# Optimization experiments

Hardware: AMD Instinct MI355X
Metric: run time of the kernel (lower is better)

## Reference

```python
import jax, jax.numpy as jnp
import numpy as np

B, N, F, DEG = 64, 1024, 128, 8
K1, K2, K3 = 512, 256, 128  # ceil(0.5*N) cascaded pool sizes
NUM_CLASSES = 10
E = B * N * DEG

def _elu(x):
    return jnp.where(x > 0, x, jnp.expm1(x))

def gcn(x, W, b, src, dst, ev, n):
    # PyG GCNConv with improved=True: self-loop weight 2, symmetric norm
    h = x @ W
    w = ev.astype(h.dtype)
    deg = jax.ops.segment_sum(w, dst, num_segments=n) + 2.0
    dinv = jax.lax.rsqrt(deg)
    coef = (w * dinv[src] * dinv[dst])[:, None]
    out = jax.ops.segment_sum(h[src] * coef, dst, num_segments=n)
    out = out + h * (2.0 * dinv * dinv)[:, None]  # self-loop term
    return out + b

def topk_pool(x, p, src, dst, ev, bg, npg, k):
    # score = tanh(x.p/||p||); keep top-k per graph; mask+remap edges
    score = jnp.tanh((x @ p) / jnp.linalg.norm(p))
    vals, idx = jax.lax.top_k(score.reshape(bg, npg), k)
    perm = (idx + (jnp.arange(bg) * npg)[:, None]).reshape(-1)
    x_new = x[perm] * vals.reshape(-1)[:, None]
    remap = jnp.full((bg * npg,), -1, jnp.int32).at[perm].set(
        jnp.arange(bg * k, dtype=jnp.int32))
    s2, d2 = remap[src], remap[dst]
    ev2 = ev & (s2 >= 0) & (d2 >= 0)
    return x_new, jnp.maximum(s2, 0), jnp.maximum(d2, 0), ev2, perm

def setup_inputs() -> dict:
    key = jax.random.key(0)
    ks = jax.random.split(key, 16)
    offs = (jnp.arange(B) * N)[:, None]
    e_per = DEG * N
    src = (jax.random.randint(ks[0], (B, e_per), 0, N) + offs).reshape(-1).astype(jnp.int32)
    dst = (jax.random.randint(ks[1], (B, e_per), 0, N) + offs).reshape(-1).astype(jnp.int32)
    def w(k, shape, fan_in):
        return jax.random.normal(k, shape, jnp.float32) / np.sqrt(fan_in)
    return {
        "x": jax.random.normal(ks[2], (B * N, F), jnp.float32),
        "W1": w(ks[3], (F, 32), F), "b1": jnp.zeros((32,)), "p1": w(ks[4], (32,), 32),
        "W2": w(ks[5], (32, 64), 32), "b2": jnp.zeros((64,)), "p2": w(ks[6], (64,), 64),
        "W3": w(ks[7], (64, 128), 64), "b3": jnp.zeros((128,)), "p3": w(ks[8], (128,), 128),
        "W4": w(ks[9], (128, 256), 128), "b4": jnp.zeros((256,)),
        "W5": w(ks[10], (384, 128), 384), "b5": jnp.zeros((128,)),
        "W6": w(ks[11], (192, 64), 192), "b6": jnp.zeros((64,)),
        "W7": w(ks[12], (96, 32), 96), "b7": jnp.zeros((32,)),
        "Wl": w(ks[13], (64, 64), 64),
        "Wc": w(ks[14], (64, NUM_CLASSES), 64), "bc": jnp.zeros((NUM_CLASSES,)),
        "src": src, "dst": dst,
    }

def reference(x, W1, b1, p1, W2, b2, p2, W3, b3, p3, W4, b4,
              W5, b5, W6, b6, W7, b7, Wl, Wc, bc, src, dst):
    ev0 = jnp.ones((E,), bool)
    x1 = _elu(gcn(x, W1, b1, src, dst, ev0, B * N))
    x2, s2, d2, ev2, idx2 = topk_pool(x1, p1, src, dst, ev0, B, N, K1)
    x2 = _elu(x2)
    x3 = _elu(gcn(x2, W2, b2, s2, d2, ev2, B * K1))
    x4, s4, d4, ev4, idx4 = topk_pool(x3, p2, s2, d2, ev2, B, K1, K2)
    x4 = _elu(x4)
    x5 = _elu(gcn(x4, W3, b3, s4, d4, ev4, B * K2))
    x6, s6, d6, ev6, idx6 = topk_pool(x5, p3, s4, d4, ev4, B, K2, K3)
    x6 = _elu(x6)
    x7 = _elu(gcn(x6, W4, b4, s6, d6, ev6, B * K3))
    x8 = jnp.zeros((B * K2, 256), x7.dtype).at[idx6].set(x7)
    x8 = _elu(jnp.concatenate([x8, x5], axis=1))
    x9 = _elu(gcn(x8, W5, b5, s4, d4, ev4, B * K2))
    x10 = jnp.zeros((B * K1, 128), x9.dtype).at[idx4].set(x9)
    x10 = _elu(jnp.concatenate([x10, x3], axis=1))
    x11 = _elu(gcn(x10, W6, b6, s2, d2, ev2, B * K1))
    x12 = jnp.zeros((B * N, 64), x11.dtype).at[idx2].set(x11)
    x12 = _elu(jnp.concatenate([x12, x1], axis=1))
    x13 = _elu(gcn(x12, W7, b7, src, dst, ev0, B * N))
    batch = jnp.repeat(jnp.arange(B), N)
    gmp = jax.ops.segment_max(x13, batch, num_segments=B)
    gap = jax.ops.segment_sum(x13, batch, num_segments=B) / N
    g = _elu(jnp.concatenate([gmp, gap], axis=1))
    g = _elu(g @ Wl)
    logits = g @ Wc + bc
    return jax.nn.log_softmax(logits, axis=-1)
```

## Files before the change

kernel.cpp:

```cpp
#include <hip/hip_runtime.h>
#include <hip/hip_bf16.h>
#include <math.h>

#define B_ 64
#define N_ 1024
#define E_ 524288
#define K1_ 512
#define K2_ 256
#define K3_ 128
#define M0_ 65536
#define M1_ 32768
#define M2_ 16384
#define M3_ 8192

static __device__ __forceinline__ float eluf(float x){ return x > 0.f ? x : expm1f(x); }
static __device__ __forceinline__ float4 elu4(float4 v){
  float4 o; o.x=eluf(v.x); o.y=eluf(v.y); o.z=eluf(v.z); o.w=eluf(v.w); return o;
}

template<int BM,int BN,int MODE>
__global__ __launch_bounds__(256) void k_mm(const float* __restrict__ X,
    const float* __restrict__ W, float* __restrict__ H, int M, int K, int N,
    const int* __restrict__ perm, const float* __restrict__ vals,
    const float* __restrict__ Xd, const int* __restrict__ orig,
    const int* __restrict__ rm, int WD4){
  constexpr int TX = BN/4;
  constexpr int TY = 256/TX;
  constexpr int RM = BM/TY;
  __shared__ float Xs[BM][36];
  __shared__ float Ws[32][BN];
  const int t = threadIdx.x;
  const int tx = t % TX, ty = t / TX;
  const int m0 = blockIdx.x*BM, n0 = blockIdx.y*BN;
  float acc[RM][4];
  #pragma unroll
  for (int r=0;r<RM;++r){acc[r][0]=0.f;acc[r][1]=0.f;acc[r][2]=0.f;acc[r][3]=0.f;}
  for (int k0=0;k0<K;k0+=32){
    #pragma unroll
    for (int l=0;l<BM/32;++l){
      int fi=l*256+t, row=fi>>3, q=fi&7;
      int m = m0+row;
      int c4 = (k0>>2)+q;
      float4 v;
      if (MODE==0){
        v = *(const float4*)(X + (size_t)m*K + (c4<<2));
      } else if (MODE==1){
        int pm = perm[m]; float vv = vals[m];
        float4 h = *(const float4*)(X + (size_t)pm*K + (c4<<2));
        v.x=eluf(h.x*vv); v.y=eluf(h.y*vv); v.z=eluf(h.z*vv); v.w=eluf(h.w*vv);
      } else {
        if (c4 < WD4){
          int o = orig ? orig[m] : m;
          int j = rm[o];
          if (j>=0) v = elu4(*(const float4*)(Xd + ((size_t)j*WD4 + c4)*4));
          else { v.x=0.f;v.y=0.f;v.z=0.f;v.w=0.f; }
        } else {
          int ws4 = (K>>2) - WD4;
          v = elu4(*(const float4*)(X + ((size_t)m*ws4 + (c4-WD4))*4));
        }
      }
      *(float4*)(&Xs[row][q*4]) = v;
    }
    #pragma unroll
    for (int l=0;l<BN/32;++l){
      int fi=l*256+t, wrow=fi/(BN/4), wq=fi%(BN/4);
      *(float4*)(&Ws[wrow][wq*4]) = *(const float4*)(W + (size_t)(k0+wrow)*N + n0 + wq*4);
    }
    __syncthreads();
    #pragma unroll
    for (int kq=0;kq<32;kq+=4){
      float4 xv[RM];
      #pragma unroll
      for (int r=0;r<RM;++r) xv[r] = *(const float4*)(&Xs[ty*RM+r][kq]);
      #pragma unroll
      for (int j=0;j<4;++j){
        float4 wv = *(const float4*)(&Ws[kq+j][tx*4]);
        #pragma unroll
        for (int r=0;r<RM;++r){
          float xs = (j==0)?xv[r].x:(j==1)?xv[r].y:(j==2)?xv[r].z:xv[r].w;
          acc[r][0]=fmaf(xs,wv.x,acc[r][0]);
          acc[r][1]=fmaf(xs,wv.y,acc[r][1]);
          acc[r][2]=fmaf(xs,wv.z,acc[r][2]);
          acc[r][3]=fmaf(xs,wv.w,acc[r][3]);
        }
      }
    }
    __syncthreads();
  }
  #pragma unroll
  for (int r=0;r<RM;++r){
    int m = m0 + ty*RM + r;
    float4 h; h.x=acc[r][0];h.y=acc[r][1];h.z=acc[r][2];h.w=acc[r][3];
    *(float4*)(H + (size_t)m*N + n0 + tx*4) = h;
  }
}

__global__ void k_deg0(const int* __restrict__ dst, int* __restrict__ degi){
  int i = blockIdx.x*256+threadIdx.x; if (i>=E_) return;
  atomicAdd(&degi[dst[i]], 1);
}
__global__ void k_place0(const int* __restrict__ src, const int* __restrict__ dst,
                         int* __restrict__ cursor, int* __restrict__ col){
  int i = blockIdx.x*256+threadIdx.x; if (i>=E_) return;
  int p = atomicAdd(&cursor[dst[i]], 1);
  col[p] = src[i];
}

__global__ __launch_bounds__(256) void k_scanA(const int* __restrict__ degi,
                                               int* __restrict__ bsum){
  __shared__ int ls[256];
  int b = blockIdx.x, t = threadIdx.x;
  ls[t] = degi[b*256+t]; __syncthreads();
  for (int o=128;o>0;o>>=1){ if (t<o) ls[t]+=ls[t+o]; __syncthreads(); }
  if (t==0) bsum[b] = ls[0];
}
__global__ __launch_bounds__(256) void k_scanB(int* __restrict__ bsum){
  __shared__ int ps[256];
  int t = threadIdx.x;
  ps[t] = bsum[t]; __syncthreads();
  for (int o=1;o<256;o<<=1){
    int v = (t>=o) ? ps[t-o] : 0;
    __syncthreads(); ps[t]+=v; __syncthreads();
  }
  bsum[t] = ps[t];
}
__global__ __launch_bounds__(256) void k_scanC(const int* __restrict__ degi,
    const int* __restrict__ bsum, int* __restrict__ rowptr,
    int* __restrict__ cursor, float* __restrict__ dinv){
  __shared__ int ps[256];
  int b = blockIdx.x, t = threadIdx.x;
  int i = b*256+t;
  int d = degi[i];
  ps[t] = d; __syncthreads();
  for (int o=1;o<256;o<<=1){
    int v = (t>=o) ? ps[t-o] : 0;
    __syncthreads(); ps[t]+=v; __syncthreads();
  }
  int off = (b==0 ? 0 : bsum[b-1]) + ps[t] - d;
  rowptr[i] = off; cursor[i] = off;
  dinv[i] = rsqrtf((float)d + 2.f);
  if (i == M0_-1) rowptr[M0_] = off + d;
}

__global__ void k_deg_orig(const int* __restrict__ orig, const int* __restrict__ rowptr0,
                           const int* __restrict__ col0, const int* __restrict__ rm,
                           float* __restrict__ dinv, int M){
  int i = blockIdx.x*256+threadIdx.x; if (i>=M) return;
  int o = orig[i];
  int beg = rowptr0[o], end = rowptr0[o+1];
  int d = 0;
  for (int j=beg;j<end;++j) d += (rm[col0[j]] >= 0) ? 1 : 0;
  dinv[i] = rsqrtf((float)d + 2.f);
}

__global__ void k_compose_idx(const int* __restrict__ prevOrig, const int* __restrict__ idxL,
                              int* __restrict__ origL, int n){
  int i = blockIdx.x*256+threadIdx.x; if (i<n) origL[i] = prevOrig[idxL[i]];
}

template<int F, bool SCORE>
__global__ __launch_bounds__(256) void k_gather(const int* __restrict__ rowptr,
    const int* __restrict__ col, const float* __restrict__ dinv,
    const float* __restrict__ H, const float* __restrict__ bias,
    float* __restrict__ OUT, int M,
    const float* __restrict__ p, float* __restrict__ score){
  constexpr int FQ = F/4;
  int i = blockIdx.x*256+threadIdx.x;
  if (i >= M*FQ) return;
  int n = i/FQ, q = i - (i/FQ)*FQ;
  int beg = rowptr[n], end = rowptr[n+1];
  float4 acc; acc.x=0.f;acc.y=0.f;acc.z=0.f;acc.w=0.f;
  for (int j=beg;j<end;++j){
    int s = col[j];
    float c = dinv[s];
    float4 h = *(const float4*)(H + (size_t)s*F + q*4);
    acc.x=fmaf(c,h.x,acc.x); acc.y=fmaf(c,h.y,acc.y);
    acc.z=fmaf(c,h.z,acc.z); acc.w=fmaf(c,h.w,acc.w);
  }
  float dn = dinv[n];
  float sc = 2.f*dn*dn;
  float4 hn = *(const float4*)(H + (size_t)n*F + q*4);
  float4 bv = *(const float4*)(bias + q*4);
  float4 o;
  o.x = eluf(fmaf(sc,hn.x,fmaf(dn,acc.x,bv.x)));
  o.y = eluf(fmaf(sc,hn.y,fmaf(dn,acc.y,bv.y)));
  o.z = eluf(fmaf(sc,hn.z,fmaf(dn,acc.z,bv.z)));
  o.w = eluf(fmaf(sc,hn.w,fmaf(dn,acc.w,bv.w)));
  *(float4*)(OUT + (size_t)n*F + q*4) = o;
  if (SCORE){
    float4 pv = *(const float4*)(p + q*4);
    float dot = o.x*pv.x + o.y*pv.y + o.z*pv.z + o.w*pv.w;
    float n2  = pv.x*pv.x + pv.y*pv.y + pv.z*pv.z + pv.w*pv.w;
    #pragma unroll
    for (int mk=FQ>>1; mk>0; mk>>=1){
      dot += __shfl_xor(dot, mk);
      n2  += __shfl_xor(n2,  mk);
    }
    if (q==0) score[n] = tanhf(dot * rsqrtf(n2));
  }
}

template<int F, bool SCORE>
__global__ __launch_bounds__(256) void k_gather_rm(const int* __restrict__ orig,
    const int* __restrict__ rowptr0, const int* __restrict__ col0,
    const int* __restrict__ rm, const float* __restrict__ dinv,
    const float* __restrict__ H, const float* __restrict__ bias,
    float* __restrict__ OUT, int M,
    const float* __restrict__ p, float* __restrict__ score){
  constexpr int FQ = F/4;
  int i = blockIdx.x*256+threadIdx.x;
  if (i >= M*FQ) return;
  int n = i/FQ, q = i - (i/FQ)*FQ;
  int o = orig[n];
  int beg = rowptr0[o], end = rowptr0[o+1];
  float4 acc; acc.x=0.f;acc.y=0.f;acc.z=0.f;acc.w=0.f;
  for (int j=beg;j<end;++j){
    int s = rm[col0[j]];
    if (s >= 0){
      float c = dinv[s];
      float4 h = *(const float4*)(H + (size_t)s*F + q*4);
      acc.x=fmaf(c,h.x,acc.x); acc.y=fmaf(c,h.y,acc.y);
      acc.z=fmaf(c,h.z,acc.z); acc.w=fmaf(c,h.w,acc.w);
    }
  }
  float dn = dinv[n];
  float sc = 2.f*dn*dn;
  float4 hn = *(const float4*)(H + (size_t)n*F + q*4);
  float4 bv = *(const float4*)(bias + q*4);
  float4 ov;
  ov.x = eluf(fmaf(sc,hn.x,fmaf(dn,acc.x,bv.x)));
  ov.y = eluf(fmaf(sc,hn.y,fmaf(dn,acc.y,bv.y)));
  ov.z = eluf(fmaf(sc,hn.z,fmaf(dn,acc.z,bv.z)));
  ov.w = eluf(fmaf(sc,hn.w,fmaf(dn,acc.w,bv.w)));
  *(float4*)(OUT + (size_t)n*F + q*4) = ov;
  if (SCORE){
    float4 pv = *(const float4*)(p + q*4);
    float dot = ov.x*pv.x + ov.y*pv.y + ov.z*pv.z + ov.w*pv.w;
    float n2  = pv.x*pv.x + pv.y*pv.y + pv.z*pv.z + pv.w*pv.w;
    #pragma unroll
    for (int mk=FQ>>1; mk>0; mk>>=1){
      dot += __shfl_xor(dot, mk);
      n2  += __shfl_xor(n2,  mk);
    }
    if (q==0) score[n] = tanhf(dot * rsqrtf(n2));
  }
}

__global__ void k_topk(const float* __restrict__ score, int npg, int K,
                       int* __restrict__ perm, float* __restrict__ vals){
  __shared__ float ss[1024]; __shared__ int si[1024];
  int g = blockIdx.x, tid = threadIdx.x;
  ss[tid] = score[g*npg + tid]; si[tid] = tid;
  __syncthreads();
  for (int k=2;k<=npg;k<<=1){
    for (int j=k>>1;j>0;j>>=1){
      int ixj = tid ^ j;
      if (ixj > tid){
        float s1=ss[tid], s2=ss[ixj]; int i1=si[tid], i2=si[ixj];
        bool aAfterB = (s1 < s2) || (s1==s2 && i1 > i2);
        bool sw = ((tid & k)==0) ? aAfterB : !aAfterB;
        if (sw){ ss[tid]=s2; si[tid]=i2; ss[ixj]=s1; si[ixj]=i1; }
      }
      __syncthreads();
    }
  }
  if (tid < K){ perm[g*K+tid] = g*npg + si[tid]; vals[g*K+tid] = ss[tid]; }
}

__global__ void k_remap_set(const int* __restrict__ perm, int* __restrict__ remap, int n){
  int i = blockIdx.x*256+threadIdx.x; if (i<n) remap[perm[i]] = i;
}

__global__ void k_head(const float* __restrict__ x13, const float* __restrict__ Wl,
                       const float* __restrict__ Wc, const float* __restrict__ bc,
                       float* __restrict__ out){
  __shared__ float smax[256], ssum[256];
  __shared__ float gv[64], g2[64], logit[10];
  int g = blockIdx.x, t = threadIdx.x;
  int f = t & 31, r0 = t >> 5;
  float mx = -3.4e38f, sm = 0.f;
  const float* base = x13 + (size_t)g*N_*32;
  for (int r=r0; r<N_; r+=8){ float v = base[r*32+f]; mx = fmaxf(mx,v); sm += v; }
  smax[t]=mx; ssum[t]=sm; __syncthreads();
  if (t<128){ smax[t]=fmaxf(smax[t],smax[t+128]); ssum[t]+=ssum[t+128]; } __syncthreads();
  if (t<64){ smax[t]=fmaxf(smax[t],smax[t+64]); ssum[t]+=ssum[t+64]; } __syncthreads();
  if (t<32){
    float m2 = fmaxf(smax[t],smax[t+32]); float s2 = ssum[t]+ssum[t+32];
    gv[t] = eluf(m2); gv[32+t] = eluf(s2 * (1.f/N_));
  }
  __syncthreads();
  if (t<64){
    float acc=0.f;
    #pragma unroll
    for (int i2=0;i2<64;++i2) acc = fmaf(gv[i2], Wl[i2*64+t], acc);
    g2[t] = eluf(acc);
  }
  __syncthreads();
  if (t<10){
    float acc = bc[t];
    #pragma unroll
    for (int j=0;j<64;++j) acc = fmaf(g2[j], Wc[j*10+t], acc);
    logit[t] = acc;
  }
  __syncthreads();
  if (t==0){
    float m=-3.4e38f; for (int c=0;c<10;++c) m=fmaxf(m,logit[c]);
    float s=0.f; for (int c=0;c<10;++c) s += expf(logit[c]-m);
    float lse = m + logf(s);
    for (int c=0;c<10;++c) out[g*10+c] = logit[c]-lse;
  }
}

extern "C" void kernel_launch(void* const* d_in, const int* in_sizes, int n_in,
                              void* d_out, int out_size, void* d_ws, size_t ws_size,
                              hipStream_t stream){
  const float* x  = (const float*)d_in[0];
  const float* W1 = (const float*)d_in[1];
  const float* b1 = (const float*)d_in[2];
  const float* p1 = (const float*)d_in[3];
  const float* W2 = (const float*)d_in[4];
  const float* b2 = (const float*)d_in[5];
  const float* p2 = (const float*)d_in[6];
  const float* W3 = (const float*)d_in[7];
  const float* b3 = (const float*)d_in[8];
  const float* p3 = (const float*)d_in[9];
  const float* W4 = (const float*)d_in[10];
  const float* b4 = (const float*)d_in[11];
  const float* W5 = (const float*)d_in[12];
  const float* b5 = (const float*)d_in[13];
  const float* W6 = (const float*)d_in[14];
  const float* b6 = (const float*)d_in[15];
  const float* W7 = (const float*)d_in[16];
  const float* b7 = (const float*)d_in[17];
  const float* Wl = (const float*)d_in[18];
  const float* Wc = (const float*)d_in[19];
  const float* bc = (const float*)d_in[20];
  const int* src0 = (const int*)d_in[21];
  const int* dst0 = (const int*)d_in[22];
  float* out = (float*)d_out;

  char* wsp = (char*)d_ws;
  size_t off = 0;
  auto alloc = [&](size_t bytes)->char*{
    char* p = wsp + off;
    off += (bytes + 255) & ~(size_t)255;
    return p;
  };
  float* bufA = (float*)alloc((size_t)2097152*4);
  float* bufB = (float*)alloc((size_t)2097152*4);
  float* bufC = (float*)alloc((size_t)2097152*4);
  float* bufD = (float*)alloc((size_t)2097152*4);
  float* bufH = (float*)alloc((size_t)2097152*4);
  float* score= (float*)alloc((size_t)M0_*4);
  float* vals2= (float*)alloc((size_t)M1_*4);
  float* vals4= (float*)alloc((size_t)M2_*4);
  float* vals6= (float*)alloc((size_t)M3_*4);
  int* idx2 = (int*)alloc((size_t)M1_*4);
  int* idx4 = (int*)alloc((size_t)M2_*4);
  int* idx6 = (int*)alloc((size_t)M3_*4);
  int* orig4 = (int*)alloc((size_t)M2_*4);
  int* orig6 = (int*)alloc((size_t)M3_*4);
  int* rm02 = (int*)alloc((size_t)M0_*4);
  int* rm04 = (int*)alloc((size_t)M0_*4);
  int* rm06 = (int*)alloc((size_t)M0_*4);
  int* col0 = (int*)alloc((size_t)E_*4);
  int* rowptr0 = (int*)alloc((size_t)(M0_+1)*4);
  int* cursor0 = (int*)alloc((size_t)M0_*4);
  int* degi0 = (int*)alloc((size_t)M0_*4);
  int* bsum  = (int*)alloc((size_t)256*4);
  float* dinv0 = (float*)alloc((size_t)M0_*4);
  float* dinv2 = (float*)alloc((size_t)M1_*4);
  float* dinv4 = (float*)alloc((size_t)M2_*4);
  float* dinv6 = (float*)alloc((size_t)M3_*4);

  auto NB = [](int total){ return (total+255)/256; };

  hipMemsetAsync(degi0, 0, (size_t)M0_*4, stream);
  k_deg0<<<NB(E_),256,0,stream>>>(dst0, degi0);
  k_scanA<<<256,256,0,stream>>>(degi0, bsum);
  k_scanB<<<1,256,0,stream>>>(bsum);
  k_scanC<<<256,256,0,stream>>>(degi0, bsum, rowptr0, cursor0, dinv0);
  k_place0<<<NB(E_),256,0,stream>>>(src0, dst0, cursor0, col0);

  k_mm<64,32,0><<<dim3(M0_/64,1),256,0,stream>>>(x, W1, bufH, M0_, 128, 32,
      nullptr,nullptr,nullptr,nullptr,nullptr,0);
  k_gather<32,true><<<NB(M0_*8),256,0,stream>>>(rowptr0, col0, dinv0, bufH, b1, bufA, M0_, p1, score);

  k_topk<<<B_,1024,0,stream>>>(score, 1024, K1_, idx2, vals2);
  hipMemsetAsync(rm02, 0xFF, (size_t)M0_*4, stream);
  k_remap_set<<<NB(M1_),256,0,stream>>>(idx2, rm02, M1_);
  k_deg_orig<<<NB(M1_),256,0,stream>>>(idx2, rowptr0, col0, rm02, dinv2, M1_);

  k_mm<64,32,1><<<dim3(M1_/64,2),256,0,stream>>>(bufA, W2, bufH, M1_, 32, 64,
      idx2, vals2, nullptr,nullptr,nullptr,0);
  k_gather_rm<64,true><<<NB(M1_*16),256,0,stream>>>(idx2, rowptr0, col0, rm02, dinv2, bufH, b2, bufB, M1_, p2, score);

  k_topk<<<B_,512,0,stream>>>(score, 512, K2_, idx4, vals4);
  k_compose_idx<<<NB(M2_),256,0,stream>>>(idx2, idx4, orig4, M2_);
  hipMemsetAsync(rm04, 0xFF, (size_t)M0_*4, stream);
  k_remap_set<<<NB(M2_),256,0,stream>>>(orig4, rm04, M2_);
  k_deg_orig<<<NB(M2_),256,0,stream>>>(orig4, rowptr0, col0, rm04, dinv4, M2_);

  k_mm<64,32,1><<<dim3(M2_/64,4),256,0,stream>>>(bufB, W3, bufH, M2_, 64, 128,
      idx4, vals4, nullptr,nullptr,nullptr,0);
  k_gather_rm<128,true><<<NB(M2_*32),256,0,stream>>>(orig4, rowptr0, col0, rm04, dinv4, bufH, b3, bufC, M2_, p3, score);

  k_topk<<<B_,256,0,stream>>>(score, 256, K3_, idx6, vals6);
  k_compose_idx<<<NB(M3_),256,0,stream>>>(orig4, idx6, orig6, M3_);
  hipMemsetAsync(rm06, 0xFF, (size_t)M0_*4, stream);
  k_remap_set<<<NB(M3_),256,0,stream>>>(orig6, rm06, M3_);
  k_deg_orig<<<NB(M3_),256,0,stream>>>(orig6, rowptr0, col0, rm06, dinv6, M3_);

  k_mm<64,32,1><<<dim3(M3_/64,8),256,0,stream>>>(bufC, W4, bufH, M3_, 128, 256,
      idx6, vals6, nullptr,nullptr,nullptr,0);
  k_gather_rm<256,false><<<NB(M3_*64),256,0,stream>>>(orig6, rowptr0, col0, rm06, dinv6, bufH, b4, bufD, M3_, nullptr, nullptr);

  k_mm<64,32,2><<<dim3(M2_/64,4),256,0,stream>>>(bufC, W5, bufH, M2_, 384, 128,
      nullptr,nullptr, bufD, orig4, rm06, 64);
  k_gather_rm<128,false><<<NB(M2_*32),256,0,stream>>>(orig4, rowptr0, col0, rm04, dinv4, bufH, b5, bufD, M2_, nullptr, nullptr);

  k_mm<64,32,2><<<dim3(M1_/64,2),256,0,stream>>>(bufB, W6, bufH, M1_, 192, 64,
      nullptr,nullptr, bufD, idx2, rm04, 32);
  k_gather_rm<64,false><<<NB(M1_*16),256,0,stream>>>(idx2, rowptr0, col0, rm02, dinv2, bufH, b6, bufC, M1_, nullptr, nullptr);

  k_mm<64,32,2><<<dim3(M0_/64,1),256,0,stream>>>(bufA, W7, bufH, M0_, 96, 32,
      nullptr,nullptr, bufC, nullptr, rm02, 16);
  k_gather<32,false><<<NB(M0_*8),256,0,stream>>>(rowptr0, col0, dinv0, bufH, b7, bufA, M0_, nullptr, nullptr);

  k_head<<<B_,256,0,stream>>>(bufA, Wl, Wc, bc, out);

  (void)in_sizes; (void)n_in; (void)out_size; (void)ws_size;
}
```

Measured before the change: 401.4 us.

## Fuse decoder GCN aggregation into next layer's matmul tile loads

Three decoder GCN gathers (layers 4, 5, 6) are removed. Their neighbor aggregation, bias and double ELU are now computed inside the following matmul's shared-memory tile load (k_mm3), so the intermediate aggregated activations are never written to or read back from memory. The remap and compose-index kernels are merged into one k_book kernel, and several matmul tile shapes change (BN 32→64, BM 128 for the first layer). The cost of the fusion is that each element is aggregated once per output column block, so the work is redundant when gridDim.y > 1. The aggregation loops also run serially inside the tile-load phase, which can lower latency hiding.

```diff
diff --git a/kernel.cpp b/kernel.cpp
--- a/kernel.cpp
+++ b/kernel.cpp
@@ -21,9 +21,7 @@
 template<int BM,int BN,int MODE>
 __global__ __launch_bounds__(256) void k_mm(const float* __restrict__ X,
     const float* __restrict__ W, float* __restrict__ H, int M, int K, int N,
-    const int* __restrict__ perm, const float* __restrict__ vals,
-    const float* __restrict__ Xd, const int* __restrict__ orig,
-    const int* __restrict__ rm, int WD4){
+    const int* __restrict__ perm, const float* __restrict__ vals){
   constexpr int TX = BN/4;
   constexpr int TY = 256/TX;
   constexpr int RM = BM/TY;
@@ -44,20 +42,10 @@
       float4 v;
       if (MODE==0){
         v = *(const float4*)(X + (size_t)m*K + (c4<<2));
-      } else if (MODE==1){
+      } else {
         int pm = perm[m]; float vv = vals[m];
         float4 h = *(const float4*)(X + (size_t)pm*K + (c4<<2));
         v.x=eluf(h.x*vv); v.y=eluf(h.y*vv); v.z=eluf(h.z*vv); v.w=eluf(h.w*vv);
-      } else {
-        if (c4 < WD4){
-          int o = orig ? orig[m] : m;
-          int j = rm[o];
-          if (j>=0) v = elu4(*(const float4*)(Xd + ((size_t)j*WD4 + c4)*4));
-          else { v.x=0.f;v.y=0.f;v.z=0.f;v.w=0.f; }
-        } else {
-          int ws4 = (K>>2) - WD4;
-          v = elu4(*(const float4*)(X + ((size_t)m*ws4 + (c4-WD4))*4));
-        }
       }
       *(float4*)(&Xs[row][q*4]) = v;
     }
@@ -95,6 +83,99 @@
   }
 }
 
+template<int BM,int BN>
+__global__ __launch_bounds__(256) void k_mm3(const float* __restrict__ Xskip,
+    const float* __restrict__ W, float* __restrict__ H, int M, int K, int N,
+    const int* __restrict__ origC,
+    const int* __restrict__ rmN,
+    const int* __restrict__ origP,
+    const int* __restrict__ rmP,
+    const float* __restrict__ dinvP, const float* __restrict__ Hp,
+    const float* __restrict__ bp,
+    const int* __restrict__ rowptr0, const int* __restrict__ col0,
+    int WD4, int NP){
+  constexpr int TX = BN/4;
+  constexpr int TY = 256/TX;
+  constexpr int RM = BM/TY;
+  __shared__ float Xs[BM][36];
+  __shared__ float Ws[32][BN];
+  const int t = threadIdx.x;
+  const int tx = t % TX, ty = t / TX;
+  const int m0 = blockIdx.x*BM, n0 = blockIdx.y*BN;
+  float acc[RM][4];
+  #pragma unroll
+  for (int r=0;r<RM;++r){acc[r][0]=0.f;acc[r][1]=0.f;acc[r][2]=0.f;acc[r][3]=0.f;}
+  for (int k0=0;k0<K;k0+=32){
+    #pragma unroll
+    for (int l=0;l<BM/32;++l){
+      int fi=l*256+t, row=fi>>3, q=fi&7;
+      int m = m0+row;
+      int c4 = (k0>>2)+q;
+      float4 v; v.x=0.f;v.y=0.f;v.z=0.f;v.w=0.f;
+      if (c4 < WD4){
+        int o = origC ? origC[m] : m;
+        int j = rmN[o];
+        if (j>=0){
+          int oj = origP[j];
+          int beg=rowptr0[oj], end=rowptr0[oj+1];
+          float4 a; a.x=0.f;a.y=0.f;a.z=0.f;a.w=0.f;
+          for (int e=beg;e<end;++e){
+            int s = rmP[col0[e]];
+            if (s>=0){
+              float c = dinvP[s];
+              float4 h = *(const float4*)(Hp + (size_t)s*NP + (c4<<2));
+              a.x=fmaf(c,h.x,a.x); a.y=fmaf(c,h.y,a.y);
+              a.z=fmaf(c,h.z,a.z); a.w=fmaf(c,h.w,a.w);
+            }
+          }
+          float dn = dinvP[j]; float sc = 2.f*dn*dn;
+          float4 hj = *(const float4*)(Hp + (size_t)j*NP + (c4<<2));
+          float4 bv = *(const float4*)(bp + (c4<<2));
+          v.x = eluf(eluf(fmaf(sc,hj.x,fmaf(dn,a.x,bv.x))));
+          v.y = eluf(eluf(fmaf(sc,hj.y,fmaf(dn,a.y,bv.y))));
+          v.z = eluf(eluf(fmaf(sc,hj.z,fmaf(dn,a.z,bv.z))));
+          v.w = eluf(eluf(fmaf(sc,hj.w,fmaf(dn,a.w,bv.w))));
+        }
+      } else {
+        int ws4 = (K>>2) - WD4;
+        v = elu4(*(const float4*)(Xskip + ((size_t)m*ws4 + (c4-WD4))*4));
+      }
+      *(float4*)(&Xs[row][q*4]) = v;
+    }
+    #pragma unroll
+    for (int l=0;l<BN/32;++l){
+      int fi=l*256+t, wrow=fi/(BN/4), wq=fi%(BN/4);
+      *(float4*)(&Ws[wrow][wq*4]) = *(const float4*)(W + (size_t)(k0+wrow)*N + n0 + wq*4);
+    }
+    __syncthreads();
+    #pragma unroll
+    for (int kq=0;kq<32;kq+=4){
+      float4 xv[RM];
+      #pragma unroll
+      for (int r=0;r<RM;++r) xv[r] = *(const float4*)(&Xs[ty*RM+r][kq]);
+      #pragma unroll
+      for (int j=0;j<4;++j){
+        float4 wv = *(const float4*)(&Ws[kq+j][tx*4]);
+        #pragma unroll
+        for (int r=0;r<RM;++r){
+          float xs = (j==0)?xv[r].x:(j==1)?xv[r].y:(j==2)?xv[r].z:xv[r].w;
+          acc[r][0]=fmaf(xs,wv.x,acc[r][0]);
+          acc[r][1]=fmaf(xs,wv.y,acc[r][1]);
+          acc[r][2]=fmaf(xs,wv.z,acc[r][2]);
+          acc[r][3]=fmaf(xs,wv.w,acc[r][3]);
+        }
+      }
+    }
+    __syncthreads();
+  }
+  #pragma unroll
+  for (int r=0;r<RM;++r){
+    int m = m0 + ty*RM + r;
+    float4 h; h.x=acc[r][0];h.y=acc[r][1];h.z=acc[r][2];h.w=acc[r][3];
+    *(float4*)(H + (size_t)m*N + n0 + tx*4) = h;
+  }
+}
+
 __global__ void k_deg0(const int* __restrict__ dst, int* __restrict__ degi){
   int i = blockIdx.x*256+threadIdx.x; if (i>=E_) return;
   atomicAdd(&degi[dst[i]], 1);
@@ -142,6 +223,13 @@
   if (i == M0_-1) rowptr[M0_] = off + d;
 }
 
+__global__ void k_book(const int* __restrict__ prevOrig, const int* __restrict__ idxL,
+                       int* __restrict__ origL, int* __restrict__ rm, int n){
+  int i = blockIdx.x*256+threadIdx.x; if (i>=n) return;
+  int o = prevOrig ? prevOrig[idxL[i]] : idxL[i];
+  origL[i] = o; rm[o] = i;
+}
+
 __global__ void k_deg_orig(const int* __restrict__ orig, const int* __restrict__ rowptr0,
                            const int* __restrict__ col0, const int* __restrict__ rm,
                            float* __restrict__ dinv, int M){
@@ -151,11 +239,6 @@
   int d = 0;
   for (int j=beg;j<end;++j) d += (rm[col0[j]] >= 0) ? 1 : 0;
   dinv[i] = rsqrtf((float)d + 2.f);
-}
-
-__global__ void k_compose_idx(const int* __restrict__ prevOrig, const int* __restrict__ idxL,
-                              int* __restrict__ origL, int n){
-  int i = blockIdx.x*256+threadIdx.x; if (i<n) origL[i] = prevOrig[idxL[i]];
 }
 
 template<int F, bool SCORE>
@@ -265,10 +348,6 @@
     }
   }
   if (tid < K){ perm[g*K+tid] = g*npg + si[tid]; vals[g*K+tid] = ss[tid]; }
-}
-
-__global__ void k_remap_set(const int* __restrict__ perm, int* __restrict__ remap, int n){
-  int i = blockIdx.x*256+threadIdx.x; if (i<n) remap[perm[i]] = i;
 }
 
 __global__ void k_head(const float* __restrict__ x13, const float* __restrict__ Wl,
@@ -349,8 +428,8 @@
   float* bufA = (float*)alloc((size_t)2097152*4);
   float* bufB = (float*)alloc((size_t)2097152*4);
   float* bufC = (float*)alloc((size_t)2097152*4);
-  float* bufD = (float*)alloc((size_t)2097152*4);
-  float* bufH = (float*)alloc((size_t)2097152*4);
+  float* Ha   = (float*)alloc((size_t)2097152*4);
+  float* Hb   = (float*)alloc((size_t)2097152*4);
   float* score= (float*)alloc((size_t)M0_*4);
   float* vals2= (float*)alloc((size_t)M1_*4);
   float* vals4= (float*)alloc((size_t)M2_*4);
@@ -382,52 +461,43 @@
   k_scanC<<<256,256,0,stream>>>(degi0, bsum, rowptr0, cursor0, dinv0);
   k_place0<<<NB(E_),256,0,stream>>>(src0, dst0, cursor0, col0);
 
-  k_mm<64,32,0><<<dim3(M0_/64,1),256,0,stream>>>(x, W1, bufH, M0_, 128, 32,
-      nullptr,nullptr,nullptr,nullptr,nullptr,0);
-  k_gather<32,true><<<NB(M0_*8),256,0,stream>>>(rowptr0, col0, dinv0, bufH, b1, bufA, M0_, p1, score);
+  k_mm<128,32,0><<<dim3(M0_/128,1),256,0,stream>>>(x, W1, Ha, M0_, 128, 32, nullptr,nullptr);
+  k_gather<32,true><<<NB(M0_*8),256,0,stream>>>(rowptr0, col0, dinv0, Ha, b1, bufA, M0_, p1, score);
 
   k_topk<<<B_,1024,0,stream>>>(score, 1024, K1_, idx2, vals2);
   hipMemsetAsync(rm02, 0xFF, (size_t)M0_*4, stream);
-  k_remap_set<<<NB(M1_),256,0,stream>>>(idx2, rm02, M1_);
+  k_book<<<NB(M1_),256,0,stream>>>(nullptr, idx2, idx2, rm02, M1_);
   k_deg_orig<<<NB(M1_),256,0,stream>>>(idx2, rowptr0, col0, rm02, dinv2, M1_);
 
-  k_mm<64,32,1><<<dim3(M1_/64,2),256,0,stream>>>(bufA, W2, bufH, M1_, 32, 64,
-      idx2, vals2, nullptr,nullptr,nullptr,0);
-  k_gather_rm<64,true><<<NB(M1_*16),256,0,stream>>>(idx2, rowptr0, col0, rm02, dinv2, bufH, b2, bufB, M1_, p2, score);
+  k_mm<64,64,1><<<dim3(M1_/64,1),256,0,stream>>>(bufA, W2, Ha, M1_, 32, 64, idx2, vals2);
+  k_gather_rm<64,true><<<NB(M1_*16),256,0,stream>>>(idx2, rowptr0, col0, rm02, dinv2, Ha, b2, bufB, M1_, p2, score);
 
   k_topk<<<B_,512,0,stream>>>(score, 512, K2_, idx4, vals4);
-  k_compose_idx<<<NB(M2_),256,0,stream>>>(idx2, idx4, orig4, M2_);
   hipMemsetAsync(rm04, 0xFF, (size_t)M0_*4, stream);
-  k_remap_set<<<NB(M2_),256,0,stream>>>(orig4, rm04, M2_);
+  k_book<<<NB(M2_),256,0,stream>>>(idx2, idx4, orig4, rm04, M2_);
   k_deg_orig<<<NB(M2_),256,0,stream>>>(orig4, rowptr0, col0, rm04, dinv4, M2_);
 
-  k_mm<64,32,1><<<dim3(M2_/64,4),256,0,stream>>>(bufB, W3, bufH, M2_, 64, 128,
-      idx4, vals4, nullptr,nullptr,nullptr,0);
-  k_gather_rm<128,true><<<NB(M2_*32),256,0,stream>>>(orig4, rowptr0, col0, rm04, dinv4, bufH, b3, bufC, M2_, p3, score);
+  k_mm<64,64,1><<<dim3(M2_/64,2),256,0,stream>>>(bufB, W3, Ha, M2_, 64, 128, idx4, vals4);
+  k_gather_rm<128,true><<<NB(M2_*32),256,0,stream>>>(orig4, rowptr0, col0, rm04, dinv4, Ha, b3, bufC, M2_, p3, score);
 
   k_topk<<<B_,256,0,stream>>>(score, 256, K3_, idx6, vals6);
-  k_compose_idx<<<NB(M3_),256,0,stream>>>(orig4, idx6, orig6, M3_);
   hipMemsetAsync(rm06, 0xFF, (size_t)M0_*4, stream);
-  k_remap_set<<<NB(M3_),256,0,stream>>>(orig6, rm06, M3_);
+  k_book<<<NB(M3_),256,0,stream>>>(orig4, idx6, orig6, rm06, M3_);
   k_deg_orig<<<NB(M3_),256,0,stream>>>(orig6, rowptr0, col0, rm06, dinv6, M3_);
 
-  k_mm<64,32,1><<<dim3(M3_/64,8),256,0,stream>>>(bufC, W4, bufH, M3_, 128, 256,
-      idx6, vals6, nullptr,nullptr,nullptr,0);
-  k_gather_rm<256,false><<<NB(M3_*64),256,0,stream>>>(orig6, rowptr0, col0, rm06, dinv6, bufH, b4, bufD, M3_, nullptr, nullptr);
-
-  k_mm<64,32,2><<<dim3(M2_/64,4),256,0,stream>>>(bufC, W5, bufH, M2_, 384, 128,
-      nullptr,nullptr, bufD, orig4, rm06, 64);
-  k_gather_rm<128,false><<<NB(M2_*32),256,0,stream>>>(orig4, rowptr0, col0, rm04, dinv4, bufH, b5, bufD, M2_, nullptr, nullptr);
-
-  k_mm<64,32,2><<<dim3(M1_/64,2),256,0,stream>>>(bufB, W6, bufH, M1_, 192, 64,
-      nullptr,nullptr, bufD, idx2, rm04, 32);
-  k_gather_rm<64,false><<<NB(M1_*16),256,0,stream>>>(idx2, rowptr0, col0, rm02, dinv2, bufH, b6, bufC, M1_, nullptr, nullptr);
-
-  k_mm<64,32,2><<<dim3(M0_/64,1),256,0,stream>>>(bufA, W7, bufH, M0_, 96, 32,
-      nullptr,nullptr, bufC, nullptr, rm02, 16);
-  k_gather<32,false><<<NB(M0_*8),256,0,stream>>>(rowptr0, col0, dinv0, bufH, b7, bufA, M0_, nullptr, nullptr);
-
-  k_head<<<B_,256,0,stream>>>(bufA, Wl, Wc, bc, out);
+  k_mm<64,64,1><<<dim3(M3_/64,4),256,0,stream>>>(bufC, W4, Ha, M3_, 128, 256, idx6, vals6);
+
+  k_mm3<64,64><<<dim3(M2_/64,2),256,0,stream>>>(bufC, W5, Hb, M2_, 384, 128,
+      orig4, rm06, orig6, rm06, dinv6, Ha, b4, rowptr0, col0, 64, 256);
+
+  k_mm3<64,64><<<dim3(M1_/64,1),256,0,stream>>>(bufB, W6, Ha, M1_, 192, 64,
+      idx2, rm04, orig4, rm04, dinv4, Hb, b5, rowptr0, col0, 32, 128);
+
+  k_mm3<64,32><<<dim3(M0_/64,1),256,0,stream>>>(bufA, W7, Hb, M0_, 96, 32,
+      nullptr, rm02, idx2, rm02, dinv2, Ha, b6, rowptr0, col0, 16, 64);
+
+  k_gather<32,false><<<NB(M0_*8),256,0,stream>>>(rowptr0, col0, dinv0, Hb, b7, bufC, M0_, nullptr, nullptr);
+  k_head<<<B_,256,0,stream>>>(bufC, Wl, Wc, bc, out);
 
   (void)in_sizes; (void)n_in; (void)out_size; (void)ws_size;
 }
```

After: 540.0 us. 1.35x slower.
